# Performance work log

Measured on AMD Instinct MI355X. Metric: run time of the kernel, lower is better.

The kernel has to match this reference:

```python
import jax, jax.numpy as jnp
import numpy as np

N_HEADS = 16

def setup_inputs() -> dict:
    key = jax.random.key(0)
    ks = jax.random.split(key, 5)
    B, T, C = 4, 2048, 1024
    x = jax.random.normal(ks[0], (B, T, C), dtype=jnp.float32)
    w_qkv = jax.random.normal(ks[1], (C, 3 * C), dtype=jnp.float32) * (C ** -0.5)
    b_qkv = jnp.zeros((3 * C,), dtype=jnp.float32)
    w_proj = jax.random.normal(ks[2], (C, C), dtype=jnp.float32) * (C ** -0.5)
    b_proj = jnp.zeros((C,), dtype=jnp.float32)
    return {"x": x, "w_qkv": w_qkv, "b_qkv": b_qkv, "w_proj": w_proj, "b_proj": b_proj}


def reference(x, w_qkv, b_qkv, w_proj, b_proj):
    B, T, C = x.shape
    H = N_HEADS
    hd = C // H
    scale = hd ** -0.5
    qkv = x @ w_qkv + b_qkv                      # [B,T,3C]
    q, k, v = jnp.split(qkv, 3, axis=-1)         # each [B,T,C]
    # -> [B,H,T,hd]
    q = q.reshape(B, T, H, hd).transpose(0, 2, 1, 3)
    k = k.reshape(B, T, H, hd).transpose(0, 2, 1, 3)
    v = v.reshape(B, T, H, hd).transpose(0, 2, 1, 3)
    attn = jnp.einsum("bhqd,bhkd->bhqk", q, k) * scale
    causal = jnp.tril(jnp.ones((T, T), dtype=bool))
    attn = jnp.where(causal, attn, -jnp.inf)
    attn = jax.nn.softmax(attn, axis=-1)         # dropout p=0 in eval/reference
    out = jnp.einsum("bhqk,bhkd->bhqd", attn, v)
    out = out.transpose(0, 2, 1, 3).reshape(B, T, C)
    return out @ w_proj + b_proj
```

## Files before the change

kernel.cpp:

```cpp
#include <hip/hip_runtime.h>
#include <hip/hip_bf16.h>


typedef float f32x4 __attribute__((ext_vector_type(4)));
typedef float f32x16 __attribute__((ext_vector_type(16)));
typedef __bf16 bf16x8 __attribute__((ext_vector_type(8)));
typedef short short8v __attribute__((ext_vector_type(8)));
typedef unsigned int u32x4 __attribute__((ext_vector_type(4)));

__device__ __forceinline__ unsigned short f2bf(float f) {
  __hip_bfloat16 h = __float2bfloat16(f);
  return __builtin_bit_cast(unsigned short, h);
}

__device__ __forceinline__ void glds16(const void* g, void* l) {
  __builtin_amdgcn_global_load_lds((const __attribute__((address_space(1))) void*)g,
                                   (__attribute__((address_space(3))) void*)l, 16, 0, 0);
}

__global__ void cvt_f32_bf16_kernel(const float* __restrict__ in,
                                    unsigned short* __restrict__ out, int n) {
  int stride = gridDim.x * blockDim.x * 4;
  for (int i = (blockIdx.x * blockDim.x + threadIdx.x) * 4; i < n; i += stride) {
    float4 v = *(const float4*)(in + i);
    ushort4 o;
    o.x = f2bf(v.x); o.y = f2bf(v.y); o.z = f2bf(v.z); o.w = f2bf(v.w);
    *(ushort4*)(out + i) = o;
  }
}

__global__ void transpose_cvt_kernel(const float* __restrict__ in,
                                     unsigned short* __restrict__ out, int K, int N) {
  __shared__ unsigned short tile[32][33];
  int tx = threadIdx.x & 31, ty = threadIdx.x >> 5;
  int n0 = blockIdx.x * 32, k0 = blockIdx.y * 32;
#pragma unroll
  for (int i = 0; i < 32; i += 8)
    tile[ty + i][tx] = f2bf(in[(size_t)(k0 + ty + i) * N + n0 + tx]);
  __syncthreads();
#pragma unroll
  for (int i = 0; i < 32; i += 8)
    out[(size_t)(n0 + ty + i) * K + k0 + tx] = tile[tx][ty + i];
}

template <int OUT_F32>
__global__ __launch_bounds__(256) void gemm_bt_kernel(
    const unsigned short* __restrict__ A, const unsigned short* __restrict__ Bt,
    const float* __restrict__ bias, void* __restrict__ Cv, int M, int N, int K) {
  __shared__ unsigned short sA[3][128 * 32];
  __shared__ unsigned short sB[3][128 * 32];
  int tid = threadIdx.x;
  int lane = tid & 63, wid = tid >> 6;
  int g = lane >> 4, r16 = lane & 15;
  int m0 = blockIdx.y * 128, n0 = blockIdx.x * 128;
  int wm = wid >> 1, wn = wid & 1;
  f32x4 acc[4][4] = {};
  int srow = tid >> 2, scol = (tid & 3) * 8;
  const unsigned short* Ap0 = A + (size_t)(m0 + srow) * K + scol;
  const unsigned short* Ap1 = A + (size_t)(m0 + 64 + srow) * K + scol;
  const unsigned short* Bp0 = Bt + (size_t)(n0 + srow) * K + scol;
  const unsigned short* Bp1 = Bt + (size_t)(n0 + 64 + srow) * K + scol;

  auto STAGE = [&](int buf, int kt) {
    glds16(Ap0 + kt, &sA[buf][tid * 8]);
    glds16(Ap1 + kt, &sA[buf][2048 + tid * 8]);
    glds16(Bp0 + kt, &sB[buf][tid * 8]);
    glds16(Bp1 + kt, &sB[buf][2048 + tid * 8]);
  };

  int nt = K >> 5;
  STAGE(0, 0);
  STAGE(1, 32);
  int cur = 0;
#pragma unroll 1
  for (int t = 0; t < nt; ++t) {
    if (t + 1 < nt) {
      asm volatile("s_waitcnt vmcnt(4)" ::: "memory");
    } else {
      asm volatile("s_waitcnt vmcnt(0)" ::: "memory");
    }
    __builtin_amdgcn_s_barrier();
    __builtin_amdgcn_sched_barrier(0);
    if (t + 2 < nt) {
      int nb = cur + 2; if (nb >= 3) nb -= 3;
      STAGE(nb, (t + 2) * 32);
    }
    const unsigned short* a = sA[cur];
    const unsigned short* bb = sB[cur];
    bf16x8 af[4], bfr[4];
#pragma unroll
    for (int m = 0; m < 4; ++m)
      af[m] = *(const bf16x8*)&a[(wm * 64 + m * 16 + r16) * 32 + g * 8];
#pragma unroll
    for (int n = 0; n < 4; ++n)
      bfr[n] = *(const bf16x8*)&bb[(wn * 64 + n * 16 + r16) * 32 + g * 8];
#pragma unroll
    for (int m = 0; m < 4; ++m)
#pragma unroll
      for (int n = 0; n < 4; ++n)
        acc[m][n] = __builtin_amdgcn_mfma_f32_16x16x32_bf16(af[m], bfr[n], acc[m][n], 0, 0, 0);
    cur = cur < 2 ? cur + 1 : 0;
  }
#pragma unroll
  for (int m = 0; m < 4; ++m)
#pragma unroll
    for (int n = 0; n < 4; ++n)
#pragma unroll
      for (int r = 0; r < 4; ++r) {
        int row = m0 + wm * 64 + m * 16 + g * 4 + r;
        int col = n0 + wn * 64 + n * 16 + r16;
        float v = acc[m][n][r] + bias[col];
        if (OUT_F32)
          ((float*)Cv)[(size_t)row * N + col] = v;
        else
          ((unsigned short*)Cv)[(size_t)row * N + col] = f2bf(v);
      }
}

__global__ void transpose_v_kernel(const unsigned short* __restrict__ qkv,
                                   unsigned short* __restrict__ vT) {
  __shared__ unsigned short tl[64][80];
  int t0 = blockIdx.x * 64;
  int bh = blockIdx.y, b = bh >> 4, h = bh & 15;
  int tid = threadIdx.x;
  int row = tid >> 2, c0 = (tid & 3) * 16;
  const unsigned short* src =
      qkv + (size_t)(b * 2048 + t0 + row) * 3072 + 2048 + h * 64 + c0;
  short8v a0 = *(const short8v*)src;
  short8v a1 = *(const short8v*)(src + 8);
#pragma unroll
  for (int j = 0; j < 8; ++j) tl[c0 + j][row] = (unsigned short)a0[j];
#pragma unroll
  for (int j = 0; j < 8; ++j) tl[c0 + 8 + j][row] = (unsigned short)a1[j];
  __syncthreads();
  int d = tid >> 2, tc = (tid & 3) * 16;
  unsigned short* dst = vT + (size_t)(bh * 64 + d) * 2048 + t0 + tc;
  *(short8v*)dst = *(const short8v*)&tl[d][tc];
  *(short8v*)(dst + 8) = *(const short8v*)&tl[d][tc + 8];
}

__global__ __launch_bounds__(512, 4) void attn_kernel(
    const unsigned short* __restrict__ qkv, const unsigned short* __restrict__ vT,
    unsigned short* __restrict__ ao) {
  __shared__ unsigned short sK[2][4096];
  __shared__ unsigned short sV[2][4096];
  __shared__ float lbuf[8][32];
  const int T = 2048, C3 = 3072;
  const float K1 = 23.083120654223415f;
  const float K2 = 16158.66f;
  int x = blockIdx.x;
  int xcd = x & 7, rest = x >> 3;
  int bh = xcd * 8 + (rest & 7);
  int qt = 7 - (rest >> 3);
  int b = bh >> 4, h = bh & 15;
  int tid = threadIdx.x, lane = tid & 63, w = tid >> 6;
  int l31 = lane & 31, hi = lane >> 5;

  int c = tid;
  int row = c >> 3, oct = (c & 7) ^ (row & 7);
  const unsigned short* Kb = qkv + (size_t)(b * T + row) * C3 + 1024 + h * 64 + oct * 8;
  const unsigned short* Vb = vT + (size_t)(bh * 64 + row) * 2048 + oct * 8;

  auto STAGE = [&](int buf, int kt) {
    int kv0 = kt * 64;
    glds16(Kb + (size_t)kv0 * C3, &sK[buf][c * 8]);
    glds16(Vb + kv0, &sV[buf][c * 8]);
  };

  int wq0 = qt * 256 + w * 32;

  const unsigned short* qp = qkv + (size_t)(b * T + wq0 + l31) * C3 + h * 64;
  bf16x8 qf[4];
#pragma unroll
  for (int d0 = 0; d0 < 4; ++d0)
    qf[d0] = *(const bf16x8*)(qp + d0 * 16 + hi * 8);

  u32x4 onesw = {0x3F803F80u, 0x3F803F80u, 0x3F803F80u, 0x3F803F80u};
  bf16x8 vones = __builtin_bit_cast(bf16x8, onesw);

  f32x16 o[2] = {};
  f32x16 lacc = {};

  int nkv = 4 * qt + 4;
  STAGE(0, 0);
  __syncthreads();
  int cur = 0;
#pragma unroll 1
  for (int kt = 0; kt < nkv; ++kt) {
    if (kt + 1 < nkv) STAGE(cur ^ 1, kt + 1);
    int kv0 = kt * 64;
    if (kv0 <= wq0 + 31) {
      f32x16 s[2] = {};
      __builtin_amdgcn_s_setprio(1);
#pragma unroll
      for (int d0 = 0; d0 < 4; ++d0) {
        int oc = ((d0 * 2 + hi) ^ (l31 & 7)) * 8;
        bf16x8 kf0 = *(const bf16x8*)&sK[cur][l31 * 64 + oc];
        bf16x8 kf1 = *(const bf16x8*)&sK[cur][(32 + l31) * 64 + oc];
        s[0] = __builtin_amdgcn_mfma_f32_32x32x16_bf16(kf0, qf[d0], s[0], 0, 0, 0);
        s[1] = __builtin_amdgcn_mfma_f32_32x32x16_bf16(kf1, qf[d0], s[1], 0, 0, 0);
      }
      __builtin_amdgcn_s_setprio(0);

      if (kv0 + 63 > wq0) {
        int thr = wq0 + l31 - kv0 - 4 * hi;
#pragma unroll
        for (int sub = 0; sub < 2; ++sub)
#pragma unroll
          for (int r = 0; r < 16; ++r) {
            int cc = sub * 32 + (r & 3) + 8 * (r >> 2);
            s[sub][r] = (cc <= thr) ? s[sub][r] : -3e38f;
          }
      }

      int pb[2][16];
#pragma unroll
      for (int sub = 0; sub < 2; ++sub)
#pragma unroll
        for (int r = 0; r < 16; ++r)
          pb[sub][r] = (int)fmaxf(fmaf(s[sub][r], K1, K2), 0.0f);

      unsigned int pk[2][8];
#pragma unroll
      for (int sub = 0; sub < 2; ++sub)
#pragma unroll
        for (int i = 0; i < 8; ++i)
          pk[sub][i] = __builtin_amdgcn_perm((unsigned)pb[sub][2 * i + 1],
                                             (unsigned)pb[sub][2 * i], 0x05040100u);
      unsigned int rc[2][4];
#pragma unroll
      for (int sub = 0; sub < 2; ++sub) {
        unsigned int s0 = hi ? pk[sub][0] : pk[sub][2];
        unsigned int s1 = hi ? pk[sub][1] : pk[sub][3];
        unsigned int s2 = hi ? pk[sub][4] : pk[sub][6];
        unsigned int s3 = hi ? pk[sub][5] : pk[sub][7];
        rc[sub][0] = __shfl_xor(s0, 32, 64);
        rc[sub][1] = __shfl_xor(s1, 32, 64);
        rc[sub][2] = __shfl_xor(s2, 32, 64);
        rc[sub][3] = __shfl_xor(s3, 32, 64);
      }

      __builtin_amdgcn_s_setprio(1);
#pragma unroll
      for (int sub = 0; sub < 2; ++sub)
#pragma unroll
        for (int t = 0; t < 2; ++t) {
          u32x4 av;
          av.x = hi ? rc[sub][2 * t]     : pk[sub][4 * t];
          av.y = hi ? rc[sub][2 * t + 1] : pk[sub][4 * t + 1];
          av.z = hi ? pk[sub][4 * t + 2] : rc[sub][2 * t];
          av.w = hi ? pk[sub][4 * t + 3] : rc[sub][2 * t + 1];
          bf16x8 pa = __builtin_bit_cast(bf16x8, av);
          int kvs = sub * 2 + t;
          int ocv = ((kvs * 2 + hi) ^ (l31 & 7)) * 8;
          bf16x8 vf0 = *(const bf16x8*)&sV[cur][l31 * 64 + ocv];
          bf16x8 vf1 = *(const bf16x8*)&sV[cur][(32 + l31) * 64 + ocv];
          o[0] = __builtin_amdgcn_mfma_f32_32x32x16_bf16(pa, vf0, o[0], 0, 0, 0);
          o[1] = __builtin_amdgcn_mfma_f32_32x32x16_bf16(pa, vf1, o[1], 0, 0, 0);
          lacc = __builtin_amdgcn_mfma_f32_32x32x16_bf16(pa, vones, lacc, 0, 0, 0);
        }
      __builtin_amdgcn_s_setprio(0);
    }
    __syncthreads();
    cur ^= 1;
  }

  if (l31 == 0) {
#pragma unroll
    for (int r = 0; r < 16; ++r)
      lbuf[w][(r & 3) + 8 * (r >> 2) + 4 * hi] = lacc[r];
  }
  __syncthreads();
  float inv = 1.f / lbuf[w][l31];
#pragma unroll
  for (int r = 0; r < 16; ++r) {
    int qrow = (r & 3) + 8 * (r >> 2) + 4 * hi;
    float iv = __shfl(inv, qrow, 64);
    size_t base = (size_t)(b * T + wq0 + qrow) * 1024 + h * 64 + l31;
    ao[base] = f2bf(o[0][r] * iv);
    ao[base + 32] = f2bf(o[1][r] * iv);
  }
}

extern "C" void kernel_launch(void* const* d_in, const int* in_sizes, int n_in,
                              void* d_out, int out_size, void* d_ws, size_t ws_size,
                              hipStream_t stream) {
  const float* x      = (const float*)d_in[0];
  const float* w_qkv  = (const float*)d_in[1];
  const float* b_qkv  = (const float*)d_in[2];
  const float* w_proj = (const float*)d_in[3];
  const float* b_proj = (const float*)d_in[4];
  float* out = (float*)d_out;

  char* ws = (char*)d_ws;
  unsigned short* xb     = (unsigned short*)(ws);
  unsigned short* ao     = (unsigned short*)(ws);
  unsigned short* wqkvT  = (unsigned short*)(ws + (16u << 20));
  unsigned short* wprojT = (unsigned short*)(ws + (22u << 20));
  unsigned short* qkv    = (unsigned short*)(ws + (24u << 20));
  unsigned short* vT     = (unsigned short*)(ws + (72u << 20));

  cvt_f32_bf16_kernel<<<2048, 256, 0, stream>>>(x, xb, 8192 * 1024);
  transpose_cvt_kernel<<<dim3(3072 / 32, 1024 / 32), 256, 0, stream>>>(w_qkv, wqkvT, 1024, 3072);
  transpose_cvt_kernel<<<dim3(1024 / 32, 1024 / 32), 256, 0, stream>>>(w_proj, wprojT, 1024, 1024);

  gemm_bt_kernel<0><<<dim3(3072 / 128, 8192 / 128), 256, 0, stream>>>(
      xb, wqkvT, b_qkv, (void*)qkv, 8192, 3072, 1024);

  transpose_v_kernel<<<dim3(32, 64), 256, 0, stream>>>(qkv, vT);

  attn_kernel<<<dim3(512), 512, 0, stream>>>(qkv, vT, ao);

  gemm_bt_kernel<1><<<dim3(1024 / 128, 8192 / 128), 256, 0, stream>>>(
      ao, wprojT, b_proj, (void*)out, 8192, 1024, 1024);
}
```

Baseline: 178.1 us.

## Enlarge GEMM tiles to 256x128 with 8 waves, split-phase pipelining and XCD remap

```diff
diff --git a/kernel.cpp b/kernel.cpp
--- a/kernel.cpp
+++ b/kernel.cpp
@@ -44,72 +44,96 @@
 }
 
 template <int OUT_F32>
-__global__ __launch_bounds__(256) void gemm_bt_kernel(
+__global__ __launch_bounds__(512, 2) void gemm_bt_kernel(
     const unsigned short* __restrict__ A, const unsigned short* __restrict__ Bt,
     const float* __restrict__ bias, void* __restrict__ Cv, int M, int N, int K) {
-  __shared__ unsigned short sA[3][128 * 32];
-  __shared__ unsigned short sB[3][128 * 32];
+  __shared__ unsigned short sA[3][256 * 32];
+  __shared__ unsigned short sB[2][128 * 32];
   int tid = threadIdx.x;
   int lane = tid & 63, wid = tid >> 6;
   int g = lane >> 4, r16 = lane & 15;
-  int m0 = blockIdx.y * 128, n0 = blockIdx.x * 128;
-  int wm = wid >> 1, wn = wid & 1;
-  f32x4 acc[4][4] = {};
+
+  int gx = gridDim.x;
+  int d = blockIdx.y * gx + blockIdx.x;
+  int cpx = (gx * gridDim.y) >> 3;
+  int nid = (d & 7) * cpx + (d >> 3);
+  int m0 = (nid / gx) * 256, n0 = (nid % gx) * 128;
+
+  int wm = wid >> 2, wn = wid & 3;
+  f32x4 acc[8][2] = {};
+
   int srow = tid >> 2, scol = (tid & 3) * 8;
   const unsigned short* Ap0 = A + (size_t)(m0 + srow) * K + scol;
-  const unsigned short* Ap1 = A + (size_t)(m0 + 64 + srow) * K + scol;
-  const unsigned short* Bp0 = Bt + (size_t)(n0 + srow) * K + scol;
-  const unsigned short* Bp1 = Bt + (size_t)(n0 + 64 + srow) * K + scol;
-
-  auto STAGE = [&](int buf, int kt) {
-    glds16(Ap0 + kt, &sA[buf][tid * 8]);
-    glds16(Ap1 + kt, &sA[buf][2048 + tid * 8]);
-    glds16(Bp0 + kt, &sB[buf][tid * 8]);
-    glds16(Bp1 + kt, &sB[buf][2048 + tid * 8]);
+  const unsigned short* Ap1 = A + (size_t)(m0 + 128 + srow) * K + scol;
+  const unsigned short* Bp = Bt + (size_t)(n0 + srow) * K + scol;
+
+  auto STAGE_A = [&](int slot, int kt) {
+    glds16(Ap0 + kt * 32, &sA[slot][tid * 8]);
+    glds16(Ap1 + kt * 32, &sA[slot][4096 + tid * 8]);
   };
+  auto STAGE_B = [&](int slot, int kt) {
+    glds16(Bp + kt * 32, &sB[slot][tid * 8]);
+  };
 
   int nt = K >> 5;
-  STAGE(0, 0);
-  STAGE(1, 32);
-  int cur = 0;
+  STAGE_A(0, 0);
+  STAGE_B(0, 0);
+  STAGE_A(1, 1);
+  asm volatile("s_waitcnt vmcnt(2)" ::: "memory");
+  __builtin_amdgcn_s_barrier();
+
+  int slA = 0;
 #pragma unroll 1
   for (int t = 0; t < nt; ++t) {
-    if (t + 1 < nt) {
-      asm volatile("s_waitcnt vmcnt(4)" ::: "memory");
+    const unsigned short* a = sA[slA];
+    const unsigned short* bb = sB[t & 1];
+    bf16x8 af[4], bfr[2];
+#pragma unroll
+    for (int mf = 0; mf < 4; ++mf)
+      af[mf] = *(const bf16x8*)&a[(wm * 128 + mf * 16 + r16) * 32 + g * 8];
+#pragma unroll
+    for (int nf = 0; nf < 2; ++nf)
+      bfr[nf] = *(const bf16x8*)&bb[(wn * 32 + nf * 16 + r16) * 32 + g * 8];
+    if (t + 1 < nt) STAGE_B((t + 1) & 1, t + 1);
+    __builtin_amdgcn_s_barrier();
+    __builtin_amdgcn_s_setprio(1);
+#pragma unroll
+    for (int mf = 0; mf < 4; ++mf)
+#pragma unroll
+      for (int nf = 0; nf < 2; ++nf)
+        acc[mf][nf] = __builtin_amdgcn_mfma_f32_16x16x32_bf16(af[mf], bfr[nf], acc[mf][nf], 0, 0, 0);
+    __builtin_amdgcn_s_setprio(0);
+    bf16x8 ag[4];
+#pragma unroll
+    for (int mf = 0; mf < 4; ++mf)
+      ag[mf] = *(const bf16x8*)&a[(wm * 128 + (mf + 4) * 16 + r16) * 32 + g * 8];
+    if (t + 2 < nt) {
+      int ns = slA + 2; if (ns >= 3) ns -= 3;
+      STAGE_A(ns, t + 2);
+      asm volatile("s_waitcnt vmcnt(2)" ::: "memory");
     } else {
       asm volatile("s_waitcnt vmcnt(0)" ::: "memory");
     }
     __builtin_amdgcn_s_barrier();
-    __builtin_amdgcn_sched_barrier(0);
-    if (t + 2 < nt) {
-      int nb = cur + 2; if (nb >= 3) nb -= 3;
-      STAGE(nb, (t + 2) * 32);
-    }
-    const unsigned short* a = sA[cur];
-    const unsigned short* bb = sB[cur];
-    bf16x8 af[4], bfr[4];
-#pragma unroll
-    for (int m = 0; m < 4; ++m)
-      af[m] = *(const bf16x8*)&a[(wm * 64 + m * 16 + r16) * 32 + g * 8];
-#pragma unroll
-    for (int n = 0; n < 4; ++n)
-      bfr[n] = *(const bf16x8*)&bb[(wn * 64 + n * 16 + r16) * 32 + g * 8];
-#pragma unroll
-    for (int m = 0; m < 4; ++m)
-#pragma unroll
-      for (int n = 0; n < 4; ++n)
-        acc[m][n] = __builtin_amdgcn_mfma_f32_16x16x32_bf16(af[m], bfr[n], acc[m][n], 0, 0, 0);
-    cur = cur < 2 ? cur + 1 : 0;
-  }
-#pragma unroll
-  for (int m = 0; m < 4; ++m)
-#pragma unroll
-    for (int n = 0; n < 4; ++n)
+    __builtin_amdgcn_s_setprio(1);
+#pragma unroll
+    for (int mf = 0; mf < 4; ++mf)
+#pragma unroll
+      for (int nf = 0; nf < 2; ++nf)
+        acc[mf + 4][nf] = __builtin_amdgcn_mfma_f32_16x16x32_bf16(ag[mf], bfr[nf], acc[mf + 4][nf], 0, 0, 0);
+    __builtin_amdgcn_s_setprio(0);
+    slA = slA == 2 ? 0 : slA + 1;
+  }
+
+#pragma unroll
+  for (int mf = 0; mf < 8; ++mf)
+#pragma unroll
+    for (int nf = 0; nf < 2; ++nf)
 #pragma unroll
       for (int r = 0; r < 4; ++r) {
-        int row = m0 + wm * 64 + m * 16 + g * 4 + r;
-        int col = n0 + wn * 64 + n * 16 + r16;
-        float v = acc[m][n][r] + bias[col];
+        int row = m0 + wm * 128 + mf * 16 + g * 4 + r;
+        int col = n0 + wn * 32 + nf * 16 + r16;
+        float v = acc[mf][nf][r] + bias[col];
         if (OUT_F32)
           ((float*)Cv)[(size_t)row * N + col] = v;
         else
@@ -133,10 +157,10 @@
 #pragma unroll
   for (int j = 0; j < 8; ++j) tl[c0 + 8 + j][row] = (unsigned short)a1[j];
   __syncthreads();
-  int d = tid >> 2, tc = (tid & 3) * 16;
-  unsigned short* dst = vT + (size_t)(bh * 64 + d) * 2048 + t0 + tc;
-  *(short8v*)dst = *(const short8v*)&tl[d][tc];
-  *(short8v*)(dst + 8) = *(const short8v*)&tl[d][tc + 8];
+  int dd = tid >> 2, tc = (tid & 3) * 16;
+  unsigned short* dst = vT + (size_t)(bh * 64 + dd) * 2048 + t0 + tc;
+  *(short8v*)dst = *(const short8v*)&tl[dd][tc];
+  *(short8v*)(dst + 8) = *(const short8v*)&tl[dd][tc + 8];
 }
 
 __global__ __launch_bounds__(512, 4) void attn_kernel(
@@ -304,13 +328,13 @@
   transpose_cvt_kernel<<<dim3(3072 / 32, 1024 / 32), 256, 0, stream>>>(w_qkv, wqkvT, 1024, 3072);
   transpose_cvt_kernel<<<dim3(1024 / 32, 1024 / 32), 256, 0, stream>>>(w_proj, wprojT, 1024, 1024);
 
-  gemm_bt_kernel<0><<<dim3(3072 / 128, 8192 / 128), 256, 0, stream>>>(
+  gemm_bt_kernel<0><<<dim3(3072 / 128, 8192 / 256), 512, 0, stream>>>(
       xb, wqkvT, b_qkv, (void*)qkv, 8192, 3072, 1024);
 
   transpose_v_kernel<<<dim3(32, 64), 256, 0, stream>>>(qkv, vT);
 
   attn_kernel<<<dim3(512), 512, 0, stream>>>(qkv, vT, ao);
 
-  gemm_bt_kernel<1><<<dim3(1024 / 128, 8192 / 128), 256, 0, stream>>>(
+  gemm_bt_kernel<1><<<dim3(1024 / 128, 8192 / 256), 512, 0, stream>>>(
       ao, wprojT, b_proj, (void*)out, 8192, 1024, 1024);
 }
```

After: 175.5 us. Within noise of the previous version (-1.5%).
